# Kernel optimization log

Hardware: AMD Instinct MI355X
Metric: run time of the kernel (lower is better)

The kernel has to match this reference:

```python
import jax, jax.numpy as jnp
import numpy as np

B, N, D = 2, 1024, 128
H = D // 2  # edge_importance hidden width


def setup_inputs() -> dict:
    key = jax.random.key(0)
    k0, k1, k2, k3, k4 = jax.random.split(key, 5)
    node_embeddings = jax.random.normal(k0, (B, N, D), dtype=jnp.float32)
    visited = jax.random.randint(k1, (B, N), 0, 2).astype(bool)
    remaining_capacity = jax.random.uniform(k2, (B, 1), dtype=jnp.float32)
    # edge_importance: Linear(2D -> H) -> ReLU -> Linear(H -> 1)
    W1 = jax.random.normal(k3, (H, 2 * D), dtype=jnp.float32) / np.sqrt(2 * D)
    b1 = jnp.zeros((H,), dtype=jnp.float32)
    W2 = jax.random.normal(k4, (1, H), dtype=jnp.float32) / np.sqrt(H)
    b2 = jnp.zeros((1,), dtype=jnp.float32)
    return {"node_embeddings": node_embeddings, "visited": visited,
            "remaining_capacity": remaining_capacity,
            "W1": W1, "b1": b1, "W2": W2, "b2": b2}


def reference(node_embeddings, visited, remaining_capacity, W1, b1, W2, b2):
    d = node_embeddings.shape[-1]
    # Linear on concat([node_i, node_j]) == split-weight sum; avoids the
    # [B,N,N,2D] concat while computing identical math.
    Wi, Wj = W1[:, :d], W1[:, d:]
    ai = jnp.einsum('bnd,hd->bnh', node_embeddings, Wi)  # [B,N,H]
    aj = jnp.einsum('bnd,hd->bnh', node_embeddings, Wj)  # [B,N,H]
    hidden = jax.nn.relu(ai[:, :, None, :] + aj[:, None, :, :] + b1)  # [B,N,N,H]
    edge_weights = jnp.einsum('bijh,oh->bij', hidden, W2) + b2[0]      # [B,N,N]
    visited_mask = visited[:, None, :] | visited[:, :, None]           # [B,N,N]
    edge_weights = jnp.where(visited_mask, jnp.float32(-1e9), edge_weights)
    adjacency = jax.nn.softmax(edge_weights, axis=-1)
    return adjacency
```

## Files before the change

kernel.cpp:

```cpp
#include <hip/hip_runtime.h>

#define Bb 2
#define Nn 1024
#define Dd 128
#define Hh 64
#define CHUNK 256
#define NCHUNK (Nn / CHUNK)
#define IT 8

__global__ __launch_bounds__(256)
void k1_proj(const float* __restrict__ E, const float* __restrict__ W1,
             const float* __restrict__ b1, float* __restrict__ Pt,
             float* __restrict__ Qt) {
  __shared__ float El[64 * 129];
  __shared__ float Wl[128 * 33];

  const int t = threadIdx.x;
  const int oBase = blockIdx.x * 32;
  const int nBase = blockIdx.y * 64;
  const int b = blockIdx.z;

  const float* esrc = E + ((size_t)b * Nn + nBase) * Dd;
  #pragma unroll
  for (int k = 0; k < 8; ++k) {
    int q = t + k * 256;
    int n = q >> 5;
    int c = (q & 31) << 2;
    float4 v = *(const float4*)(esrc + n * Dd + c);
    float* dst = &El[n * 129 + c];
    dst[0] = v.x; dst[1] = v.y; dst[2] = v.z; dst[3] = v.w;
  }
  #pragma unroll
  for (int k = 0; k < 16; ++k) {
    int q = t + k * 256;
    int o = q >> 7;
    int d = q & 127;
    int oG = oBase + o;
    int src = (oG < Hh) ? (oG * 2 * Dd + d) : ((oG - Hh) * 2 * Dd + Dd + d);
    Wl[d * 33 + o] = W1[src];
  }
  __syncthreads();

  const int tn = t & 15;
  const int to = t >> 4;
  float acc[4][2] = {{0.f, 0.f}, {0.f, 0.f}, {0.f, 0.f}, {0.f, 0.f}};
  #pragma unroll 8
  for (int d = 0; d < 128; ++d) {
    float w0 = Wl[d * 33 + to * 2 + 0];
    float w1 = Wl[d * 33 + to * 2 + 1];
    #pragma unroll
    for (int a = 0; a < 4; ++a) {
      float e = El[(tn * 4 + a) * 129 + d];
      acc[a][0] = fmaf(e, w0, acc[a][0]);
      acc[a][1] = fmaf(e, w1, acc[a][1]);
    }
  }

  #pragma unroll
  for (int j = 0; j < 2; ++j) {
    int o = oBase + to * 2 + j;
    float4 v = make_float4(acc[0][j], acc[1][j], acc[2][j], acc[3][j]);
    float* dst;
    if (o < Hh) {
      float bias = b1[o];
      v.x += bias; v.y += bias; v.z += bias; v.w += bias;
      dst = Pt + ((size_t)b * Hh + o) * Nn + nBase + tn * 4;
    } else {
      dst = Qt + ((size_t)b * Hh + (o - Hh)) * Nn + nBase + tn * 4;
    }
    *(float4*)dst = v;
  }
}

__device__ __forceinline__ void gload_lds16(const float* g, float* l) {
  __builtin_amdgcn_global_load_lds(
      (const __attribute__((address_space(1))) void*)g,
      (__attribute__((address_space(3))) void*)l, 16, 0, 0);
}

__global__ __launch_bounds__(256)
void k23_fused(const float* __restrict__ Pt, const float* __restrict__ Qt,
               const float* __restrict__ W2, const float* __restrict__ b2,
               const int* __restrict__ visited, float* __restrict__ out) {
  __shared__ float Ql[2][Hh][CHUNK];
  __shared__ float Pl[Hh][IT];

  const int t  = threadIdx.x;
  const int tx = t & 63;
  const int ty = t >> 6;
  const int iBase = blockIdx.x * IT;
  const int b  = blockIdx.y;

  #pragma unroll
  for (int k = 0; k < 2; ++k) {
    int e = t + k * 256;
    int h = e >> 3, i = e & 7;
    Pl[h][i] = Pt[((size_t)b * Hh + h) * Nn + iBase + i];
  }

  const float* qb = Qt + (size_t)b * Hh * Nn;

  auto stage = [&](int buf, int ch) {
    const int jB = ch * CHUNK;
    #pragma unroll
    for (int r = 0; r < 16; ++r) {
      const int h = ty * 16 + r;
      gload_lds16(qb + (size_t)h * Nn + jB + tx * 4, &Ql[buf][h][0]);
    }
  };

  float acc[2][16];
  #pragma unroll
  for (int k = 0; k < 16; ++k) { acc[0][k] = 0.f; acc[1][k] = 0.f; }

  stage(0, 0);
  __syncthreads();

  #pragma unroll
  for (int ch = 0; ch < NCHUNK; ++ch) {
    const int buf = ch & 1;
    if (ch + 1 < NCHUNK) stage(buf ^ 1, ch + 1);

    #pragma unroll 8
    for (int h = 0; h < Hh; ++h) {
      const float  w = W2[h];
      const float4 q = *(const float4*)&Ql[buf][h][tx * 4];
      const float p0 = Pl[h][2 * ty + 0];
      const float p1 = Pl[h][2 * ty + 1];
      const float qa[4] = {q.x, q.y, q.z, q.w};
      #pragma unroll
      for (int c = 0; c < 4; ++c) {
        acc[0][ch * 4 + c] = fmaf(w, fmaxf(p0 + qa[c], 0.f), acc[0][ch * 4 + c]);
        acc[1][ch * 4 + c] = fmaf(w, fmaxf(p1 + qa[c], 0.f), acc[1][ch * 4 + c]);
      }
    }
    __syncthreads();
  }

  const float NEG = -1000000000.0f;
  const float b2v = b2[0];
  const int vrow = b * Nn;
  const bool vi0 = visited[vrow + iBase + 2 * ty + 0] != 0;
  const bool vi1 = visited[vrow + iBase + 2 * ty + 1] != 0;

  float m0 = NEG, m1 = NEG;
  #pragma unroll
  for (int ch = 0; ch < NCHUNK; ++ch) {
    const int4 vj = *(const int4*)(visited + vrow + ch * CHUNK + tx * 4);
    const int vja[4] = {vj.x, vj.y, vj.z, vj.w};
    #pragma unroll
    for (int c = 0; c < 4; ++c) {
      const bool mj = vja[c] != 0;
      float v0 = (vi0 | mj) ? NEG : (acc[0][ch * 4 + c] + b2v);
      float v1 = (vi1 | mj) ? NEG : (acc[1][ch * 4 + c] + b2v);
      acc[0][ch * 4 + c] = v0;
      acc[1][ch * 4 + c] = v1;
      m0 = fmaxf(m0, v0);
      m1 = fmaxf(m1, v1);
    }
  }
  #pragma unroll
  for (int off = 32; off; off >>= 1) {
    m0 = fmaxf(m0, __shfl_xor(m0, off));
    m1 = fmaxf(m1, __shfl_xor(m1, off));
  }

  float s0 = 0.f, s1 = 0.f;
  #pragma unroll
  for (int k = 0; k < 16; ++k) {
    const float e0 = __expf(acc[0][k] - m0);
    const float e1 = __expf(acc[1][k] - m1);
    acc[0][k] = e0; acc[1][k] = e1;
    s0 += e0; s1 += e1;
  }
  #pragma unroll
  for (int off = 32; off; off >>= 1) {
    s0 += __shfl_xor(s0, off);
    s1 += __shfl_xor(s1, off);
  }
  const float i0 = 1.0f / s0, i1 = 1.0f / s1;

  float* o0 = out + (size_t)(b * Nn + iBase + 2 * ty + 0) * Nn;
  float* o1 = out + (size_t)(b * Nn + iBase + 2 * ty + 1) * Nn;
  #pragma unroll
  for (int ch = 0; ch < NCHUNK; ++ch) {
    const int j = ch * CHUNK + tx * 4;
    float4 w0 = make_float4(acc[0][ch * 4 + 0] * i0, acc[0][ch * 4 + 1] * i0,
                            acc[0][ch * 4 + 2] * i0, acc[0][ch * 4 + 3] * i0);
    float4 w1 = make_float4(acc[1][ch * 4 + 0] * i1, acc[1][ch * 4 + 1] * i1,
                            acc[1][ch * 4 + 2] * i1, acc[1][ch * 4 + 3] * i1);
    *(float4*)(o0 + j) = w0;
    *(float4*)(o1 + j) = w1;
  }
}

extern "C" void kernel_launch(void* const* d_in, const int* in_sizes, int n_in,
                              void* d_out, int out_size, void* d_ws, size_t ws_size,
                              hipStream_t stream) {
  const float* E       = (const float*)d_in[0];
  const int*   visited = (const int*)d_in[1];
  const float* W1      = (const float*)d_in[3];
  const float* b1      = (const float*)d_in[4];
  const float* W2      = (const float*)d_in[5];
  const float* b2      = (const float*)d_in[6];

  float* out = (float*)d_out;
  float* Pt  = (float*)d_ws;
  float* Qt  = (float*)((char*)d_ws + (size_t)Bb * Hh * Nn * sizeof(float));

  k1_proj<<<dim3(4, 16, Bb), 256, 0, stream>>>(E, W1, b1, Pt, Qt);
  k23_fused<<<dim3(Nn / IT, Bb), 256, 0, stream>>>(Pt, Qt, W2, b2, visited, out);
}
```

Before: 94.71 us.

## Restructure fused edge kernel: 4 rows per block, 512 threads, direct Q loads

The fused scoring and softmax kernel now handles 4 output rows per block with 512 threads, each thread owning 2 columns. The LDS double-buffered Q staging is dropped in favour of register-prefetched float2 global loads. Softmax max and sum become cross-wave reductions through small shared arrays. The aim is more blocks, lower register pressure and better occupancy. The cost is that each Q element is reused across only 4 rows instead of 8, so Q traffic doubles, and each row needs extra block-level syncs.

```diff
diff --git a/kernel.cpp b/kernel.cpp
--- a/kernel.cpp
+++ b/kernel.cpp
@@ -4,9 +4,6 @@
 #define Nn 1024
 #define Dd 128
 #define Hh 64
-#define CHUNK 256
-#define NCHUNK (Nn / CHUNK)
-#define IT 8
 
 __global__ __launch_bounds__(256)
 void k1_proj(const float* __restrict__ E, const float* __restrict__ W1,
@@ -72,125 +69,118 @@
   }
 }
 
-__device__ __forceinline__ void gload_lds16(const float* g, float* l) {
-  __builtin_amdgcn_global_load_lds(
-      (const __attribute__((address_space(1))) void*)g,
-      (__attribute__((address_space(3))) void*)l, 16, 0, 0);
-}
-
-__global__ __launch_bounds__(256)
+__global__ __launch_bounds__(512)
 void k23_fused(const float* __restrict__ Pt, const float* __restrict__ Qt,
                const float* __restrict__ W2, const float* __restrict__ b2,
                const int* __restrict__ visited, float* __restrict__ out) {
-  __shared__ float Ql[2][Hh][CHUNK];
-  __shared__ float Pl[Hh][IT];
-
-  const int t  = threadIdx.x;
-  const int tx = t & 63;
-  const int ty = t >> 6;
-  const int iBase = blockIdx.x * IT;
-  const int b  = blockIdx.y;
-
-  #pragma unroll
-  for (int k = 0; k < 2; ++k) {
-    int e = t + k * 256;
-    int h = e >> 3, i = e & 7;
-    Pl[h][i] = Pt[((size_t)b * Hh + h) * Nn + iBase + i];
-  }
-
-  const float* qb = Qt + (size_t)b * Hh * Nn;
-
-  auto stage = [&](int buf, int ch) {
-    const int jB = ch * CHUNK;
-    #pragma unroll
-    for (int r = 0; r < 16; ++r) {
-      const int h = ty * 16 + r;
-      gload_lds16(qb + (size_t)h * Nn + jB + tx * 4, &Ql[buf][h][0]);
+  __shared__ float Pl[Hh][4];
+  __shared__ float Ml[4][8];
+  __shared__ float Sl[4][8];
+
+  const int t    = threadIdx.x;
+  const int lane = t & 63;
+  const int wv   = t >> 6;
+  const int iBase = blockIdx.x * 4;
+  const int b    = blockIdx.y;
+
+  if (t < 256) {
+    const int h = t >> 2, r = t & 3;
+    Pl[h][r] = Pt[((size_t)b * Hh + h) * Nn + iBase + r];
+  }
+  __syncthreads();
+
+  const int jOff = wv * 128 + lane * 2;
+  const float* qcol = Qt + (size_t)b * Hh * Nn + jOff;
+
+  float acc[4][2];
+  #pragma unroll
+  for (int r = 0; r < 4; ++r) { acc[r][0] = 0.f; acc[r][1] = 0.f; }
+
+  float2 qn = *(const float2*)qcol;
+  #pragma unroll 8
+  for (int h = 0; h < Hh; ++h) {
+    const float2 q = qn;
+    if (h + 1 < Hh) qn = *(const float2*)(qcol + (size_t)(h + 1) * Nn);
+    const float w = W2[h];
+    const float4 p4 = *(const float4*)&Pl[h][0];
+    const float p[4] = {p4.x, p4.y, p4.z, p4.w};
+    const float qa[2] = {q.x, q.y};
+    #pragma unroll
+    for (int r = 0; r < 4; ++r) {
+      acc[r][0] = fmaf(w, fmaxf(p[r] + qa[0], 0.f), acc[r][0]);
+      acc[r][1] = fmaf(w, fmaxf(p[r] + qa[1], 0.f), acc[r][1]);
     }
-  };
-
-  float acc[2][16];
-  #pragma unroll
-  for (int k = 0; k < 16; ++k) { acc[0][k] = 0.f; acc[1][k] = 0.f; }
-
-  stage(0, 0);
-  __syncthreads();
-
-  #pragma unroll
-  for (int ch = 0; ch < NCHUNK; ++ch) {
-    const int buf = ch & 1;
-    if (ch + 1 < NCHUNK) stage(buf ^ 1, ch + 1);
-
-    #pragma unroll 8
-    for (int h = 0; h < Hh; ++h) {
-      const float  w = W2[h];
-      const float4 q = *(const float4*)&Ql[buf][h][tx * 4];
-      const float p0 = Pl[h][2 * ty + 0];
-      const float p1 = Pl[h][2 * ty + 1];
-      const float qa[4] = {q.x, q.y, q.z, q.w};
-      #pragma unroll
-      for (int c = 0; c < 4; ++c) {
-        acc[0][ch * 4 + c] = fmaf(w, fmaxf(p0 + qa[c], 0.f), acc[0][ch * 4 + c]);
-        acc[1][ch * 4 + c] = fmaf(w, fmaxf(p1 + qa[c], 0.f), acc[1][ch * 4 + c]);
-      }
-    }
-    __syncthreads();
   }
 
   const float NEG = -1000000000.0f;
   const float b2v = b2[0];
   const int vrow = b * Nn;
-  const bool vi0 = visited[vrow + iBase + 2 * ty + 0] != 0;
-  const bool vi1 = visited[vrow + iBase + 2 * ty + 1] != 0;
-
-  float m0 = NEG, m1 = NEG;
-  #pragma unroll
-  for (int ch = 0; ch < NCHUNK; ++ch) {
-    const int4 vj = *(const int4*)(visited + vrow + ch * CHUNK + tx * 4);
-    const int vja[4] = {vj.x, vj.y, vj.z, vj.w};
-    #pragma unroll
-    for (int c = 0; c < 4; ++c) {
-      const bool mj = vja[c] != 0;
-      float v0 = (vi0 | mj) ? NEG : (acc[0][ch * 4 + c] + b2v);
-      float v1 = (vi1 | mj) ? NEG : (acc[1][ch * 4 + c] + b2v);
-      acc[0][ch * 4 + c] = v0;
-      acc[1][ch * 4 + c] = v1;
-      m0 = fmaxf(m0, v0);
-      m1 = fmaxf(m1, v1);
-    }
-  }
-  #pragma unroll
-  for (int off = 32; off; off >>= 1) {
-    m0 = fmaxf(m0, __shfl_xor(m0, off));
-    m1 = fmaxf(m1, __shfl_xor(m1, off));
-  }
-
-  float s0 = 0.f, s1 = 0.f;
-  #pragma unroll
-  for (int k = 0; k < 16; ++k) {
-    const float e0 = __expf(acc[0][k] - m0);
-    const float e1 = __expf(acc[1][k] - m1);
-    acc[0][k] = e0; acc[1][k] = e1;
-    s0 += e0; s1 += e1;
-  }
-  #pragma unroll
-  for (int off = 32; off; off >>= 1) {
-    s0 += __shfl_xor(s0, off);
-    s1 += __shfl_xor(s1, off);
-  }
-  const float i0 = 1.0f / s0, i1 = 1.0f / s1;
-
-  float* o0 = out + (size_t)(b * Nn + iBase + 2 * ty + 0) * Nn;
-  float* o1 = out + (size_t)(b * Nn + iBase + 2 * ty + 1) * Nn;
-  #pragma unroll
-  for (int ch = 0; ch < NCHUNK; ++ch) {
-    const int j = ch * CHUNK + tx * 4;
-    float4 w0 = make_float4(acc[0][ch * 4 + 0] * i0, acc[0][ch * 4 + 1] * i0,
-                            acc[0][ch * 4 + 2] * i0, acc[0][ch * 4 + 3] * i0);
-    float4 w1 = make_float4(acc[1][ch * 4 + 0] * i1, acc[1][ch * 4 + 1] * i1,
-                            acc[1][ch * 4 + 2] * i1, acc[1][ch * 4 + 3] * i1);
-    *(float4*)(o0 + j) = w0;
-    *(float4*)(o1 + j) = w1;
+
+  bool vi[4];
+  #pragma unroll
+  for (int r = 0; r < 4; ++r) vi[r] = visited[vrow + iBase + r] != 0;
+
+  const int2 vj = *(const int2*)(visited + vrow + jOff);
+  const bool mj0 = vj.x != 0, mj1 = vj.y != 0;
+
+  float vv[4][2];
+  float m[4];
+  #pragma unroll
+  for (int r = 0; r < 4; ++r) {
+    float x0 = (vi[r] | mj0) ? NEG : acc[r][0] + b2v;
+    float x1 = (vi[r] | mj1) ? NEG : acc[r][1] + b2v;
+    vv[r][0] = x0; vv[r][1] = x1;
+    m[r] = fmaxf(x0, x1);
+  }
+  #pragma unroll
+  for (int off = 32; off; off >>= 1)
+    #pragma unroll
+    for (int r = 0; r < 4; ++r)
+      m[r] = fmaxf(m[r], __shfl_xor(m[r], off));
+  if (lane == 0) {
+    #pragma unroll
+    for (int r = 0; r < 4; ++r) Ml[r][wv] = m[r];
+  }
+  __syncthreads();
+  #pragma unroll
+  for (int r = 0; r < 4; ++r) {
+    const float4 a = *(const float4*)&Ml[r][0];
+    const float4 c = *(const float4*)&Ml[r][4];
+    m[r] = fmaxf(fmaxf(fmaxf(a.x, a.y), fmaxf(a.z, a.w)),
+                 fmaxf(fmaxf(c.x, c.y), fmaxf(c.z, c.w)));
+  }
+
+  float e[4][2];
+  float s[4];
+  #pragma unroll
+  for (int r = 0; r < 4; ++r) {
+    e[r][0] = __expf(vv[r][0] - m[r]);
+    e[r][1] = __expf(vv[r][1] - m[r]);
+    s[r] = e[r][0] + e[r][1];
+  }
+  #pragma unroll
+  for (int off = 32; off; off >>= 1)
+    #pragma unroll
+    for (int r = 0; r < 4; ++r)
+      s[r] += __shfl_xor(s[r], off);
+  if (lane == 0) {
+    #pragma unroll
+    for (int r = 0; r < 4; ++r) Sl[r][wv] = s[r];
+  }
+  __syncthreads();
+  #pragma unroll
+  for (int r = 0; r < 4; ++r) {
+    const float4 a = *(const float4*)&Sl[r][0];
+    const float4 c = *(const float4*)&Sl[r][4];
+    s[r] = ((a.x + a.y) + (a.z + a.w)) + ((c.x + c.y) + (c.z + c.w));
+  }
+
+  #pragma unroll
+  for (int r = 0; r < 4; ++r) {
+    const float inv = 1.0f / s[r];
+    float* orow = out + ((size_t)(b * Nn + iBase + r)) * Nn + jOff;
+    float2 vout = make_float2(e[r][0] * inv, e[r][1] * inv);
+    *(float2*)orow = vout;
   }
 }
 
@@ -209,5 +199,5 @@
   float* Qt  = (float*)((char*)d_ws + (size_t)Bb * Hh * Nn * sizeof(float));
 
   k1_proj<<<dim3(4, 16, Bb), 256, 0, stream>>>(E, W1, b1, Pt, Qt);
-  k23_fused<<<dim3(Nn / IT, Bb), 256, 0, stream>>>(Pt, Qt, W2, b2, visited, out);
+  k23_fused<<<dim3(Nn / 4, Bb), 512, 0, stream>>>(Pt, Qt, W2, b2, visited, out);
 }
```

Result: faster. 89.95 us (-5.0%).
